# Optimization experiments

Hardware: AMD Instinct MI355X
Metric: run time of the kernel (lower is better)

The kernel has to match this reference:

```python
import jax, jax.numpy as jnp
import numpy as np

B, S, V, D, H, L = 2, 1024, 32000, 1024, 16, 4
DK = D // H
DF = 4 * D
EPS = 1e-5


def setup_inputs() -> dict:
    key = jax.random.key(0)
    ks = jax.random.split(key, 9)
    s = 0.02
    rn = lambda k, shape: jax.random.normal(k, shape, jnp.float32) * s
    return {
        "input_ids": jax.random.randint(ks[0], (B, S), 0, V, dtype=jnp.int32),
        "emb": rn(ks[1], (V, D)),
        "Wq": rn(ks[2], (L, D, D)),
        "Wk": rn(ks[3], (L, D, D)),
        "Wv": rn(ks[4], (L, D, D)),
        "Wo": rn(ks[5], (L, D, D)),
        "W1": rn(ks[6], (L, D, DF)),
        "b1": jnp.zeros((L, DF), jnp.float32),
        "W2": rn(ks[7], (L, DF, D)),
        "b2": jnp.zeros((L, D), jnp.float32),
        "ln1_g": jnp.ones((L, D), jnp.float32),
        "ln1_b": jnp.zeros((L, D), jnp.float32),
        "ln2_g": jnp.ones((L, D), jnp.float32),
        "ln2_b": jnp.zeros((L, D), jnp.float32),
        "lnf_g": jnp.ones((D,), jnp.float32),
        "lnf_b": jnp.zeros((D,), jnp.float32),
        "head_w": rn(ks[8], (D, V)),
    }


def _ln(x, g, b):
    m = jnp.mean(x, -1, keepdims=True)
    v = jnp.mean(jnp.square(x - m), -1, keepdims=True)
    return (x - m) * jax.lax.rsqrt(v + EPS) * g + b


def _heads(x):
    # [B,S,D] -> [B,H,S,DK]
    return x.reshape(B, S, H, DK).transpose(0, 2, 1, 3)


def _forward(input_ids, emb, Wq, Wk, Wv, Wo, W1, b1, W2, b2,
             ln1_g, ln1_b, ln2_g, ln2_b, lnf_g, lnf_b, head_w):
    x = emb[input_ids]  # [B,S,D]
    # causal mask: position q attends to k <= q (prefill, no past)
    mask = jnp.triu(jnp.full((S, S), -jnp.inf, jnp.float32), k=1)
    scale = 1.0 / np.sqrt(DK).astype(np.float32)

    def block(x, p):
        wq, wk, wv, wo, w1, bb1, w2, bb2, g1, be1, g2, be2 = p
        h = _ln(x, g1, be1)
        q = _heads(h @ wq)
        k = _heads(h @ wk)
        v = _heads(h @ wv)
        scores = jnp.einsum('bhqd,bhkd->bhqk', q, k) * scale + mask
        a = jax.nn.softmax(scores, axis=-1)
        o = jnp.einsum('bhqk,bhkd->bhqd', a, v)
        o = o.transpose(0, 2, 1, 3).reshape(B, S, D) @ wo
        x = x + o
        h2 = _ln(x, g2, be2)
        x = x + jax.nn.gelu(h2 @ w1 + bb1, approximate=False) @ w2 + bb2
        return x, None

    x, _ = jax.lax.scan(block, x, (Wq, Wk, Wv, Wo, W1, b1, W2, b2,
                                   ln1_g, ln1_b, ln2_g, ln2_b))
    logits = _ln(x, lnf_g, lnf_b) @ head_w  # [B,S,V]
    return logits


def reference(input_ids, emb, Wq, Wk, Wv, Wo, W1, b1, W2, b2,
              ln1_g, ln1_b, ln2_g, ln2_b, lnf_g, lnf_b, head_w):
    return _forward(input_ids, emb, Wq, Wk, Wv, Wo, W1, b1, W2, b2,
                    ln1_g, ln1_b, ln2_g, ln2_b, lnf_g, lnf_b, head_w)
```

## Files before the change

### kernel.cpp

```cpp
#include <hip/hip_runtime.h>
#include <stdint.h>

#define B_ 2
#define S_ 1024
#define V_ 32000
#define D_ 1024
#define H_ 16
#define L_ 4
#define DF_ 4096
#define M_ (B_*S_)

typedef short short8 __attribute__((ext_vector_type(8)));
typedef float f32x4 __attribute__((ext_vector_type(4)));

__device__ __forceinline__ unsigned short f2bf(float f){
  union { float f; unsigned int u; } v; v.f = f;
  unsigned int u = v.u;
  u = u + 0x7fffu + ((u >> 16) & 1u);
  return (unsigned short)(u >> 16);
}

__device__ __forceinline__ void gload16(const void* g, void* l){
  __builtin_amdgcn_global_load_lds(
      (__attribute__((address_space(1))) void*)(uintptr_t)g,
      (__attribute__((address_space(3))) void*)(uintptr_t)l, 16, 0, 0);
}

__global__ __launch_bounds__(256) void embed_k(const int* __restrict__ ids,
    const float* __restrict__ emb, float* __restrict__ x){
  int row = blockIdx.x;
  int id = ids[row];
  float4 v = reinterpret_cast<const float4*>(emb + (size_t)id*D_)[threadIdx.x];
  reinterpret_cast<float4*>(x + (size_t)row*D_)[threadIdx.x] = v;
}

__global__ __launch_bounds__(256) void ln_k(const float* __restrict__ x,
    const float* __restrict__ g, const float* __restrict__ b,
    unsigned short* __restrict__ out){
  int row = blockIdx.x;
  int tid = threadIdx.x;
  float4 v = reinterpret_cast<const float4*>(x + (size_t)row*D_)[tid];
  float s = v.x+v.y+v.z+v.w;
  float ss = v.x*v.x + v.y*v.y + v.z*v.z + v.w*v.w;
  #pragma unroll
  for (int off=1; off<64; off<<=1){ s += __shfl_xor(s, off); ss += __shfl_xor(ss, off); }
  __shared__ float rs[4], rss[4];
  int wave = tid>>6, lane = tid&63;
  if (lane==0){ rs[wave]=s; rss[wave]=ss; }
  __syncthreads();
  s  = rs[0]+rs[1]+rs[2]+rs[3];
  ss = rss[0]+rss[1]+rss[2]+rss[3];
  float mean = s * (1.0f/(float)D_);
  float var  = ss * (1.0f/(float)D_) - mean*mean;
  float inv = rsqrtf(var + 1e-5f);
  float4 gg = reinterpret_cast<const float4*>(g)[tid];
  float4 bb = reinterpret_cast<const float4*>(b)[tid];
  ushort4 o;
  o.x = f2bf((v.x-mean)*inv*gg.x + bb.x);
  o.y = f2bf((v.y-mean)*inv*gg.y + bb.y);
  o.z = f2bf((v.z-mean)*inv*gg.z + bb.z);
  o.w = f2bf((v.w-mean)*inv*gg.w + bb.w);
  reinterpret_cast<ushort4*>(out + (size_t)row*D_)[tid] = o;
}

__global__ __launch_bounds__(256) void rln_k(float* __restrict__ x,
    const float* __restrict__ part, const float* __restrict__ bias,
    const float* __restrict__ g, const float* __restrict__ b,
    unsigned short* __restrict__ out, int KS){
  int row = blockIdx.x;
  int tid = threadIdx.x;
  float4 v = reinterpret_cast<const float4*>(x + (size_t)row*D_)[tid];
  for (int z=0; z<KS; z++){
    float4 p = reinterpret_cast<const float4*>(part + (size_t)z*M_*D_ + (size_t)row*D_)[tid];
    v.x+=p.x; v.y+=p.y; v.z+=p.z; v.w+=p.w;
  }
  if (bias){
    float4 bb4 = reinterpret_cast<const float4*>(bias)[tid];
    v.x+=bb4.x; v.y+=bb4.y; v.z+=bb4.z; v.w+=bb4.w;
  }
  reinterpret_cast<float4*>(x + (size_t)row*D_)[tid] = v;
  float s = v.x+v.y+v.z+v.w;
  float ss = v.x*v.x + v.y*v.y + v.z*v.z + v.w*v.w;
  #pragma unroll
  for (int off=1; off<64; off<<=1){ s += __shfl_xor(s, off); ss += __shfl_xor(ss, off); }
  __shared__ float rs[4], rss[4];
  int wave = tid>>6, lane = tid&63;
  if (lane==0){ rs[wave]=s; rss[wave]=ss; }
  __syncthreads();
  s  = rs[0]+rs[1]+rs[2]+rs[3];
  ss = rss[0]+rss[1]+rss[2]+rss[3];
  float mean = s * (1.0f/(float)D_);
  float var  = ss * (1.0f/(float)D_) - mean*mean;
  float inv = rsqrtf(var + 1e-5f);
  float4 gg = reinterpret_cast<const float4*>(g)[tid];
  float4 bb = reinterpret_cast<const float4*>(b)[tid];
  ushort4 o;
  o.x = f2bf((v.x-mean)*inv*gg.x + bb.x);
  o.y = f2bf((v.y-mean)*inv*gg.y + bb.y);
  o.z = f2bf((v.z-mean)*inv*gg.z + bb.z);
  o.w = f2bf((v.w-mean)*inv*gg.w + bb.w);
  reinterpret_cast<ushort4*>(out + (size_t)row*D_)[tid] = o;
}

__global__ __launch_bounds__(256) void transpose_k(const float* __restrict__ in,
    unsigned short* __restrict__ out, int K, int N, size_t in_ls, size_t out_ls){
  __shared__ float t[64][65];
  const float* inp = in + (size_t)blockIdx.z*in_ls;
  unsigned short* outp = out + (size_t)blockIdx.z*out_ls;
  int k0 = blockIdx.y*64, n0 = blockIdx.x*64;
  int rr = threadIdx.x >> 4, c4 = (threadIdx.x & 15)*4;
  #pragma unroll
  for (int i=0;i<4;i++){
    float4 v = *reinterpret_cast<const float4*>(inp + (size_t)(k0+rr+i*16)*N + n0 + c4);
    t[rr+i*16][c4+0]=v.x; t[rr+i*16][c4+1]=v.y; t[rr+i*16][c4+2]=v.z; t[rr+i*16][c4+3]=v.w;
  }
  __syncthreads();
  #pragma unroll
  for (int i=0;i<4;i++){
    int n = rr + i*16;
    ushort4 o;
    o.x = f2bf(t[c4+0][n]); o.y = f2bf(t[c4+1][n]);
    o.z = f2bf(t[c4+2][n]); o.w = f2bf(t[c4+3][n]);
    *reinterpret_cast<ushort4*>(outp + (size_t)(n0+n)*K + k0 + c4) = o;
  }
}

#define VMC(n)  asm volatile("s_waitcnt vmcnt(" #n ")" ::: "memory")

template<int EP>
__global__ __launch_bounds__(256)
void gemm_bt(const unsigned short* __restrict__ A, const unsigned short* __restrict__ B,
             void* __restrict__ C, const float* __restrict__ bias,
             const float* __restrict__ resid, int K, int ldc, int MB, int kLen){
  __shared__ unsigned short As[2][128*64];
  __shared__ unsigned short Bs[2][128*64];
  const int tid = threadIdx.x;
  const int wave = tid>>6, lane = tid&63;
  const int wm = wave>>1, wn = wave&1;
  const int nwg = gridDim.x;
  const int p = blockIdx.x;
  const int t = (nwg & 7) ? p : ((p & 7)*(nwg>>3) + (p>>3));
  const int by = t % MB, bx = t / MB;
  const int row0 = by*128, col0 = bx*128;
  const int kz = blockIdx.z;
  const int k0 = kz*kLen;
  f32x4 acc[4][4] = {};
  const int sw8 = ((lane&7) ^ ((lane>>3)&7))*8;
  const unsigned short* Ag = A + (size_t)(row0 + wave*8 + (lane>>3))*K + sw8;
  const unsigned short* Bg = B + (size_t)(col0 + wave*8 + (lane>>3))*K + sw8;
  const int r = lane&15, g16 = lane>>4;
  const int rsw = (r&7)<<4;
#define STAGE_BT(buf, kt) do{ \
    _Pragma("unroll") \
    for (int i=0;i<4;i++){ \
      gload16(Ag + (size_t)i*32*K + (kt), As[buf] + (wave*8 + i*32)*64); \
      gload16(Bg + (size_t)i*32*K + (kt), Bs[buf] + (wave*8 + i*32)*64); \
    } }while(0)
  STAGE_BT(0, k0);
  __syncthreads();
  int cur = 0;
  for (int kt=k0; kt<k0+kLen; kt+=64){
    if (kt + 64 < k0 + kLen) STAGE_BT(cur^1, kt+64);
    #pragma unroll
    for (int ks=0; ks<2; ks++){
      short8 a[4], b[4];
      #pragma unroll
      for (int m=0;m<4;m++)
        a[m] = *reinterpret_cast<const short8*>((const char*)As[cur] + (wm*64+m*16+r)*128 + ((ks*64 + g16*16) ^ rsw));
      #pragma unroll
      for (int n=0;n<4;n++)
        b[n] = *reinterpret_cast<const short8*>((const char*)Bs[cur] + (wn*64+n*16+r)*128 + ((ks*64 + g16*16) ^ rsw));
      #pragma unroll
      for (int m=0;m<4;m++)
        #pragma unroll
        for (int n=0;n<4;n++)
          acc[m][n] = __builtin_amdgcn_mfma_f32_16x16x32_bf16(a[m], b[n], acc[m][n], 0,0,0);
    }
    __syncthreads();
    cur ^= 1;
  }
  #pragma unroll
  for (int m=0;m<4;m++){
    const int row = row0 + wm*64 + m*16 + g16*4;
    #pragma unroll
    for (int n=0;n<4;n++){
      const int col = col0 + wn*64 + n*16 + r;
      #pragma unroll
      for (int j=0;j<4;j++){
        float val = acc[m][n][j];
        size_t idx = (size_t)(row+j)*ldc + col;
        if constexpr (EP==2 || EP==3) val += bias[col];
        if constexpr (EP==2) val = 0.5f*val*(1.0f + erff(val*0.70710678118f));
        if constexpr (EP==1 || EP==3) val += resid[idx];
        if constexpr (EP==0 || EP==2) ((unsigned short*)C)[idx] = f2bf(val);
        else ((float*)C)[idx] = val;
      }
    }
  }
}

#define LDA8(buf,m,ks) (*(const short8*)(lds8 + (buf)*65536 + (wm*128+(m)*16+r)*128 + (((ks)*64+g16*16)^rsw)))
#define LDB8(buf,n,ks) (*(const short8*)(lds8 + (buf)*65536 + 32768 + (wn*64+(n)*16+r)*128 + (((ks)*64+g16*16)^rsw)))
#define STG(buf,isB,h,i,tile) gload16( \
    ((isB) ? Bw + (size_t)(col0 + (h)*128 + (i)*64 + wave*8 + srow)*K + (size_t)(tile)*64 + scsw \
           : A  + (size_t)(row0 + (h)*128 + (i)*64 + wave*8 + srow)*K + (size_t)(tile)*64 + scsw), \
    lds8 + (buf)*65536 + (isB)*32768 + ((h)*128 + (i)*64 + wave*8)*128 )
#define STG_HT(buf,isB,h,tile) do{ STG(buf,isB,h,0,tile); STG(buf,isB,h,1,tile); }while(0)
#define BLOAD8(bT) do{ \
  bfr[0][0]=LDB8(bT,0,0); bfr[0][1]=LDB8(bT,0,1); bfr[1][0]=LDB8(bT,1,0); bfr[1][1]=LDB8(bT,1,1); \
  bfr[2][0]=LDB8(bT,2,0); bfr[2][1]=LDB8(bT,2,1); bfr[3][0]=LDB8(bT,3,0); bfr[3][1]=LDB8(bT,3,1); }while(0)
#define MM8(mb,n) do{ \
  acc[mb][n]    =__builtin_amdgcn_mfma_f32_16x16x32_bf16(a0[0],bfr[n][0],acc[mb][n],0,0,0); \
  acc[mb][n]    =__builtin_amdgcn_mfma_f32_16x16x32_bf16(a0[1],bfr[n][1],acc[mb][n],0,0,0); \
  acc[(mb)+1][n]=__builtin_amdgcn_mfma_f32_16x16x32_bf16(a1[0],bfr[n][0],acc[(mb)+1][n],0,0,0); \
  acc[(mb)+1][n]=__builtin_amdgcn_mfma_f32_16x16x32_bf16(a1[1],bfr[n][1],acc[(mb)+1][n],0,0,0); }while(0)
#define PH8(bT, mb, STAGES, TAIL) do{ \
  short8 a0[2], a1[2]; \
  a0[0]=LDA8(bT,mb,0); a0[1]=LDA8(bT,mb,1); a1[0]=LDA8(bT,(mb)+1,0); a1[1]=LDA8(bT,(mb)+1,1); \
  STAGES; \
  __builtin_amdgcn_s_barrier(); \
  asm volatile("s_waitcnt lgkmcnt(0)" ::: "memory"); \
  __builtin_amdgcn_s_setprio(1); \
  MM8(mb,0); MM8(mb,1); MM8(mb,2); MM8(mb,3); \
  __builtin_amdgcn_s_setprio(0); \
  TAIL; \
  __builtin_amdgcn_s_barrier(); \
}while(0)

__global__ __launch_bounds__(512, 2)
void gemm_8ph(const unsigned short* __restrict__ A, const unsigned short* __restrict__ Bw,
              float* __restrict__ C, int K, int ldc, int MB){
  __shared__ char lds8[131072];
  const int tid = threadIdx.x;
  const int wave = tid>>6, lane = tid&63;
  const int wm = wave>>2, wn = wave&3;
  const int nwg = gridDim.x;
  const int pp = blockIdx.x;
  const int t = (nwg & 7) ? pp : ((pp & 7)*(nwg>>3) + (pp>>3));
  const int by = t % MB, bx = t / MB;
  const int row0 = by*256, col0 = bx*256;
  const int r = lane&15, g16 = lane>>4;
  const int rsw = (r&7)<<4;
  const int srow = lane>>3;
  const int scsw = ((lane&7) ^ srow)*8;

  f32x4 acc[8][4] = {};
  short8 bfr[4][2];
  const int NT = K/64;

  STG_HT(0,1,0,0); STG_HT(0,1,1,0);
  STG_HT(0,0,0,0); STG_HT(0,0,1,0);
  STG_HT(1,1,0,1); STG_HT(1,1,1,1);
  VMC(4);
  __builtin_amdgcn_s_barrier();

  for (int T0 = 0; T0 < NT-2; T0 += 2){
    BLOAD8(0);
    PH8(0, 0, STG_HT(1,0,0,T0+1), ((void)0));
    PH8(0, 2, STG_HT(1,0,1,T0+1), ((void)0));
    PH8(0, 4, STG_HT(0,1,0,T0+2), ((void)0));
    PH8(0, 6, STG_HT(0,1,1,T0+2), VMC(4));
    BLOAD8(1);
    PH8(1, 0, STG_HT(0,0,0,T0+2), ((void)0));
    PH8(1, 2, STG_HT(0,0,1,T0+2), ((void)0));
    PH8(1, 4, STG_HT(1,1,0,T0+3), ((void)0));
    PH8(1, 6, STG_HT(1,1,1,T0+3), VMC(4));
  }
  BLOAD8(0);
  PH8(0, 0, STG_HT(1,0,0,NT-1), ((void)0));
  PH8(0, 2, STG_HT(1,0,1,NT-1), ((void)0));
  PH8(0, 4, ((void)0), ((void)0));
  PH8(0, 6, ((void)0), VMC(0));
  BLOAD8(1);
  PH8(1, 0, ((void)0), ((void)0));
  PH8(1, 2, ((void)0), ((void)0));
  PH8(1, 4, ((void)0), ((void)0));
  PH8(1, 6, ((void)0), ((void)0));

  #pragma unroll
  for (int m=0;m<8;m++){
    const int row = row0 + wm*128 + m*16 + g16*4;
    #pragma unroll
    for (int n=0;n<4;n++){
      const int col = col0 + wn*64 + n*16 + r;
      #pragma unroll
      for (int j=0;j<4;j++)
        C[(size_t)(row+j)*ldc + col] = acc[m][n][j];
    }
  }
}

#define L4A(buf,m,ks) (*(const short8*)(lds4 + (buf)*49152 + (wm*64+(m)*16+r)*128 + (((ks)*64+g16*16)^rsw)))
#define L4B(buf,n,ks) (*(const short8*)(lds4 + (buf)*49152 + 16384 + (wn*64+(n)*16+r)*128 + (((ks)*64+g16*16)^rsw)))
#define STG4A(buf,tile) do{ \
  gload16(A4 + (size_t)(row0 + 0*64 + wave*8 + srow)*K + (size_t)(tile)*64 + scsw, lds4 + (buf)*49152 + (0*64+wave*8)*128); \
  gload16(A4 + (size_t)(row0 + 1*64 + wave*8 + srow)*K + (size_t)(tile)*64 + scsw, lds4 + (buf)*49152 + (1*64+wave*8)*128); }while(0)
#define STG4B(buf,tile) do{ \
  gload16(B4 + (size_t)(col0 + 0*64 + wave*8 + srow)*K + (size_t)(tile)*64 + scsw, lds4 + (buf)*49152 + 16384 + (0*64+wave*8)*128); \
  gload16(B4 + (size_t)(col0 + 1*64 + wave*8 + srow)*K + (size_t)(tile)*64 + scsw, lds4 + (buf)*49152 + 16384 + (1*64+wave*8)*128); \
  gload16(B4 + (size_t)(col0 + 2*64 + wave*8 + srow)*K + (size_t)(tile)*64 + scsw, lds4 + (buf)*49152 + 16384 + (2*64+wave*8)*128); \
  gload16(B4 + (size_t)(col0 + 3*64 + wave*8 + srow)*K + (size_t)(tile)*64 + scsw, lds4 + (buf)*49152 + 16384 + (3*64+wave*8)*128); }while(0)
#define BLOAD4(bT) do{ \
  bfr4[0][0]=L4B(bT,0,0); bfr4[0][1]=L4B(bT,0,1); bfr4[1][0]=L4B(bT,1,0); bfr4[1][1]=L4B(bT,1,1); \
  bfr4[2][0]=L4B(bT,2,0); bfr4[2][1]=L4B(bT,2,1); bfr4[3][0]=L4B(bT,3,0); bfr4[3][1]=L4B(bT,3,1); }while(0)
#define MM44(mb,n) do{ \
  acc[mb][n]    =__builtin_amdgcn_mfma_f32_16x16x32_bf16(a0[0],bfr4[n][0],acc[mb][n],0,0,0); \
  acc[mb][n]    =__builtin_amdgcn_mfma_f32_16x16x32_bf16(a0[1],bfr4[n][1],acc[mb][n],0,0,0); \
  acc[(mb)+1][n]=__builtin_amdgcn_mfma_f32_16x16x32_bf16(a1[0],bfr4[n][0],acc[(mb)+1][n],0,0,0); \
  acc[(mb)+1][n]=__builtin_amdgcn_mfma_f32_16x16x32_bf16(a1[1],bfr4[n][1],acc[(mb)+1][n],0,0,0); }while(0)
#define PH4(bT, mb, STAGES, TAIL) do{ \
  short8 a0[2], a1[2]; \
  a0[0]=L4A(bT,mb,0); a0[1]=L4A(bT,mb,1); a1[0]=L4A(bT,(mb)+1,0); a1[1]=L4A(bT,(mb)+1,1); \
  STAGES; \
  __builtin_amdgcn_s_barrier(); \
  asm volatile("s_waitcnt lgkmcnt(0)" ::: "memory"); \
  __builtin_amdgcn_s_setprio(1); \
  MM44(mb,0); MM44(mb,1); MM44(mb,2); MM44(mb,3); \
  __builtin_amdgcn_s_setprio(0); \
  TAIL; \
  __builtin_amdgcn_s_barrier(); \
}while(0)

template<int EP>
__global__ __launch_bounds__(512, 2)
void gemm_4ph(const unsigned short* __restrict__ A, const unsigned short* __restrict__ Bw,
              void* __restrict__ C, const float* __restrict__ bias,
              int K, int ldc, int MB, int kLen){
  __shared__ char lds4[98304];
  const int tid = threadIdx.x;
  const int wave = tid>>6, lane = tid&63;
  const int wm = wave>>2, wn = wave&3;
  const int nwg = gridDim.x;
  const int pp = blockIdx.x;
  const int t = (nwg & 7) ? pp : ((pp & 7)*(nwg>>3) + (pp>>3));
  const int by = t % MB, bx = t / MB;
  const int row0 = by*128, col0 = bx*256;
  const int r = lane&15, g16 = lane>>4;
  const int rsw = (r&7)<<4;
  const int srow = lane>>3;
  const int scsw = ((lane&7) ^ srow)*8;
  const int kz = blockIdx.z;
  const unsigned short* A4 = A + (size_t)kz*kLen;
  const unsigned short* B4 = Bw + (size_t)kz*kLen;

  f32x4 acc[4][4] = {};
  short8 bfr4[4][2];
  const int NT = kLen/64;

  STG4B(0,0); STG4A(0,0); STG4B(1,1);
  VMC(4);
  __builtin_amdgcn_s_barrier();

  for (int T0 = 0; T0 < NT-2; T0 += 2){
    BLOAD4(0);
    PH4(0, 0, STG4A(1,T0+1), ((void)0));
    PH4(0, 2, STG4B(0,T0+2), VMC(4));
    BLOAD4(1);
    PH4(1, 0, STG4A(0,T0+2), ((void)0));
    PH4(1, 2, STG4B(1,T0+3), VMC(4));
  }
  BLOAD4(0);
  PH4(0, 0, STG4A(1,NT-1), ((void)0));
  PH4(0, 2, ((void)0), VMC(0));
  BLOAD4(1);
  PH4(1, 0, ((void)0), ((void)0));
  PH4(1, 2, ((void)0), ((void)0));

  float* Cp5 = (float*)C + (size_t)kz*M_*ldc;
  #pragma unroll
  for (int m=0;m<4;m++){
    const int row = row0 + wm*64 + m*16 + g16*4;
    #pragma unroll
    for (int n=0;n<4;n++){
      const int col = col0 + wn*64 + n*16 + r;
      #pragma unroll
      for (int j=0;j<4;j++){
        float val = acc[m][n][j];
        size_t idx = (size_t)(row+j)*ldc + col;
        if constexpr (EP==2) { val += bias[col]; val = 0.5f*val*(1.0f + erff(val*0.70710678118f)); }
        if constexpr (EP==0 || EP==2) ((unsigned short*)C)[idx] = f2bf(val);
        else Cp5[idx] = val;
      }
    }
  }
}

__global__ __launch_bounds__(256)
void attn_k(const unsigned short* __restrict__ qkv, unsigned short* __restrict__ o){
  __shared__ unsigned short Ks[64*64];
  __shared__ unsigned short Vt[64*64];
  __shared__ unsigned short Ps[4*16*64];
  const int tid = threadIdx.x;
  const int wave = tid>>6, lane = tid&63;
  const int qb = blockIdx.x, h = blockIdx.y, b = blockIdx.z;
  const int r = lane&15, g = lane>>4;
  const size_t rowbase = (size_t)b*S_*3*D_;
  short8 qf[2];
  {
    const unsigned short* qp = qkv + rowbase + (size_t)(qb*64 + wave*16 + r)*(3*D_) + h*64 + g*8;
    qf[0] = *reinterpret_cast<const short8*>(qp);
    qf[1] = *reinterpret_cast<const short8*>(qp + 32);
  }
  float mrow[4] = {-INFINITY,-INFINITY,-INFINITY,-INFINITY};
  float lrow[4] = {0.f,0.f,0.f,0.f};
  f32x4 oacc[4] = {};
  const int qglob0 = qb*64 + wave*16 + g*4;
  unsigned short* Pw = Ps + wave*16*64;

  for (int kt=0; kt<=qb; kt++){
    __syncthreads();
    #pragma unroll
    for (int i=0;i<2;i++){
      int key = i*32 + (tid>>3);
      int c8 = (tid&7)*8;
      const unsigned short* kp = qkv + rowbase + (size_t)(kt*64+key)*(3*D_) + D_ + h*64 + c8;
      uint4 kd = *reinterpret_cast<const uint4*>(kp);
      int bo = (key*128 + c8*2) ^ ((key&7)<<4);
      *reinterpret_cast<uint4*>((char*)Ks + bo) = kd;
      const unsigned short* vp = qkv + rowbase + (size_t)(kt*64+key)*(3*D_) + 2*D_ + h*64 + c8;
      uint4 vd = *reinterpret_cast<const uint4*>(vp);
      const unsigned short* ve = reinterpret_cast<const unsigned short*>(&vd);
      #pragma unroll
      for (int j=0;j<8;j++){
        int d = c8 + j;
        int bo2 = (d*128 + key*2) ^ ((d&7)<<4);
        *reinterpret_cast<unsigned short*>((char*)Vt + bo2) = ve[j];
      }
    }
    __syncthreads();
    f32x4 sacc[4] = {};
    #pragma unroll
    for (int ks=0; ks<2; ks++){
      #pragma unroll
      for (int nb=0; nb<4; nb++){
        int key = nb*16 + r;
        int bo = (key*128 + (ks*32+g*8)*2) ^ ((key&7)<<4);
        short8 kf = *reinterpret_cast<const short8*>((char*)Ks + bo);
        sacc[nb] = __builtin_amdgcn_mfma_f32_16x16x32_bf16(qf[ks], kf, sacc[nb], 0,0,0);
      }
    }
    float sv[4][4];
    float tm[4] = {-INFINITY,-INFINITY,-INFINITY,-INFINITY};
    #pragma unroll
    for (int nb=0; nb<4; nb++){
      int key = kt*64 + nb*16 + r;
      #pragma unroll
      for (int j=0;j<4;j++){
        float s = sacc[nb][j]*0.125f;
        s = (key <= qglob0 + j) ? s : -INFINITY;
        sv[nb][j] = s;
        tm[j] = fmaxf(tm[j], s);
      }
    }
    #pragma unroll
    for (int off=1; off<16; off<<=1){
      #pragma unroll
      for (int j=0;j<4;j++) tm[j] = fmaxf(tm[j], __shfl_xor(tm[j], off));
    }
    float sf[4], psum[4];
    #pragma unroll
    for (int j=0;j<4;j++){
      float mn = fmaxf(mrow[j], tm[j]);
      sf[j] = __expf(mrow[j]-mn);
      mrow[j] = mn;
      psum[j] = 0.0f;
    }
    #pragma unroll
    for (int nb=0; nb<4; nb++){
      #pragma unroll
      for (int j=0;j<4;j++){
        float p = __expf(sv[nb][j]-mrow[j]);
        psum[j] += p;
        int prow = g*4+j;
        int bo = (prow*128 + (nb*16+r)*2) ^ ((prow&7)<<4);
        *reinterpret_cast<unsigned short*>((char*)Pw + bo) = f2bf(p);
      }
    }
    #pragma unroll
    for (int off=1; off<16; off<<=1){
      #pragma unroll
      for (int j=0;j<4;j++) psum[j] += __shfl_xor(psum[j], off);
    }
    #pragma unroll
    for (int j=0;j<4;j++) lrow[j] = lrow[j]*sf[j] + psum[j];
    #pragma unroll
    for (int nb=0;nb<4;nb++){
      #pragma unroll
      for (int j=0;j<4;j++) oacc[nb][j] *= sf[j];
    }
    asm volatile("s_waitcnt lgkmcnt(0)" ::: "memory");
    #pragma unroll
    for (int ks=0; ks<2; ks++){
      int bo = (r*128 + (ks*32+g*8)*2) ^ ((r&7)<<4);
      short8 pf = *reinterpret_cast<const short8*>((char*)Pw + bo);
      #pragma unroll
      for (int nb=0; nb<4; nb++){
        int d = nb*16 + r;
        int bo2 = (d*128 + (ks*32+g*8)*2) ^ ((d&7)<<4);
        short8 vf = *reinterpret_cast<const short8*>((char*)Vt + bo2);
        oacc[nb] = __builtin_amdgcn_mfma_f32_16x16x32_bf16(pf, vf, oacc[nb], 0,0,0);
      }
    }
  }
  #pragma unroll
  for (int nb=0; nb<4; nb++){
    #pragma unroll
    for (int j=0;j<4;j++){
      float ov = oacc[nb][j] / lrow[j];
      size_t row = (size_t)b*S_ + qb*64 + wave*16 + g*4 + j;
      o[row*D_ + h*64 + nb*16 + r] = f2bf(ov);
    }
  }
}

extern "C" void kernel_launch(void* const* d_in, const int* in_sizes, int n_in,
                              void* d_out, int out_size, void* d_ws, size_t ws_size,
                              hipStream_t stream) {
  const int*   ids   = (const int*)  d_in[0];
  const float* emb   = (const float*)d_in[1];
  const float* Wq    = (const float*)d_in[2];
  const float* Wk    = (const float*)d_in[3];
  const float* Wv    = (const float*)d_in[4];
  const float* Wo    = (const float*)d_in[5];
  const float* W1    = (const float*)d_in[6];
  const float* b1    = (const float*)d_in[7];
  const float* W2    = (const float*)d_in[8];
  const float* b2    = (const float*)d_in[9];
  const float* ln1_g = (const float*)d_in[10];
  const float* ln1_b = (const float*)d_in[11];
  const float* ln2_g = (const float*)d_in[12];
  const float* ln2_b = (const float*)d_in[13];
  const float* lnf_g = (const float*)d_in[14];
  const float* lnf_b = (const float*)d_in[15];
  const float* headw = (const float*)d_in[16];

  unsigned short* ws = (unsigned short*)d_ws;
  unsigned short* wqkvT = ws;
  unsigned short* woT   = wqkvT + (size_t)L_*3*D_*D_;
  unsigned short* w1T   = woT   + (size_t)L_*D_*D_;
  unsigned short* w2T   = w1T   + (size_t)L_*D_*DF_;
  unsigned short* headT = w2T   + (size_t)L_*D_*DF_;
  unsigned short* h     = headT + (size_t)V_*D_;
  unsigned short* qkv   = h     + (size_t)M_*D_;
  unsigned short* attno = qkv   + (size_t)M_*3*D_;
  unsigned short* h2    = attno + (size_t)M_*D_;
  float*          x     = (float*)(h2 + (size_t)M_*DF_);
  float*          part  = x + (size_t)M_*D_;
  size_t needed = ((char*)(part + (size_t)4*M_*D_)) - (char*)d_ws;
  const bool splitk = (ws_size >= needed);

  transpose_k<<<dim3(D_/64, D_/64, L_), 256, 0, stream>>>(Wq, wqkvT,            D_, D_, (size_t)D_*D_, (size_t)3*D_*D_);
  transpose_k<<<dim3(D_/64, D_/64, L_), 256, 0, stream>>>(Wk, wqkvT + D_*D_,    D_, D_, (size_t)D_*D_, (size_t)3*D_*D_);
  transpose_k<<<dim3(D_/64, D_/64, L_), 256, 0, stream>>>(Wv, wqkvT + 2*D_*D_,  D_, D_, (size_t)D_*D_, (size_t)3*D_*D_);
  transpose_k<<<dim3(D_/64, D_/64, L_), 256, 0, stream>>>(Wo, woT,              D_, D_, (size_t)D_*D_, (size_t)D_*D_);
  transpose_k<<<dim3(DF_/64, D_/64, L_), 256, 0, stream>>>(W1, w1T,             D_, DF_, (size_t)D_*DF_, (size_t)D_*DF_);
  transpose_k<<<dim3(D_/64, DF_/64, L_), 256, 0, stream>>>(W2, w2T,             DF_, D_, (size_t)D_*DF_, (size_t)D_*DF_);
  transpose_k<<<dim3(V_/64, D_/64, 1), 256, 0, stream>>>(headw, headT,          D_, V_, 0, 0);

  embed_k<<<M_, 256, 0, stream>>>(ids, emb, x);
  ln_k<<<M_, 256, 0, stream>>>(x, ln1_g, ln1_b, h);

  for (int l = 0; l < L_; l++){
    gemm_4ph<0><<<dim3((3*D_/256)*(M_/128), 1, 1), 512, 0, stream>>>(h, wqkvT + (size_t)l*3*D_*D_, qkv, nullptr, D_, 3*D_, M_/128, D_);
    attn_k<<<dim3(S_/64, H_, B_), 256, 0, stream>>>(qkv, attno);
    if (splitk){
      gemm_4ph<5><<<dim3((D_/256)*(M_/128), 1, 4), 512, 0, stream>>>(attno, woT + (size_t)l*D_*D_, part, nullptr, D_, D_, M_/128, D_/4);
      rln_k<<<M_, 256, 0, stream>>>(x, part, nullptr, ln2_g + l*D_, ln2_b + l*D_, h, 4);
    } else {
      gemm_bt<1><<<dim3((D_/128)*(M_/128), 1, 1), 256, 0, stream>>>(attno, woT + (size_t)l*D_*D_, x, nullptr, x, D_, D_, M_/128, D_);
      ln_k<<<M_, 256, 0, stream>>>(x, ln2_g + l*D_, ln2_b + l*D_, h);
    }
    gemm_4ph<2><<<dim3((DF_/256)*(M_/128), 1, 1), 512, 0, stream>>>(h, w1T + (size_t)l*D_*DF_, h2, b1 + l*DF_, D_, DF_, M_/128, D_);
    const float* ng = (l+1 < L_) ? (ln1_g + (l+1)*D_) : lnf_g;
    const float* nb = (l+1 < L_) ? (ln1_b + (l+1)*D_) : lnf_b;
    if (splitk){
      gemm_4ph<5><<<dim3((D_/256)*(M_/128), 1, 4), 512, 0, stream>>>(h2, w2T + (size_t)l*D_*DF_, part, nullptr, DF_, D_, M_/128, DF_/4);
      rln_k<<<M_, 256, 0, stream>>>(x, part, b2 + l*D_, ng, nb, h, 4);
    } else {
      gemm_bt<3><<<dim3((D_/128)*(M_/128), 1, 1), 256, 0, stream>>>(h2, w2T + (size_t)l*D_*DF_, x, b2 + l*D_, x, DF_, D_, M_/128, DF_);
      ln_k<<<M_, 256, 0, stream>>>(x, ng, nb, h);
    }
  }

  gemm_8ph<<<dim3((V_/256)*(M_/256), 1, 1), 512, 0, stream>>>(h, headT, (float*)d_out, D_, V_, M_/256);
}
```

Measured before the change: 894.1 us.

## Double-buffer K/V tiles in attention and skip redundant rescaling

The attention kernel now double-buffers K and V tiles in shared memory. It prefetches the next K tile with direct global-to-LDS loads and the next V tile into registers while computing on the current tile, so the loads overlap the MFMA and softmax work. The 1/sqrt(dk) scale is folded into Q at load time, the causal mask is applied only on the diagonal tile, and the running-max rescale of the output and row sum is skipped when no row max changed. This doubles the K/V shared-memory footprint, which may lower occupancy, and rounding the scaled Q to bf16 slightly changes numerics.

```diff
diff --git a/kernel.cpp b/kernel.cpp
--- a/kernel.cpp
+++ b/kernel.cpp
@@ -18,6 +18,11 @@
   unsigned int u = v.u;
   u = u + 0x7fffu + ((u >> 16) & 1u);
   return (unsigned short)(u >> 16);
+}
+
+__device__ __forceinline__ float bf2f(unsigned short u){
+  union { unsigned int u; float f; } v; v.u = ((unsigned int)u) << 16;
+  return v.f;
 }
 
 __device__ __forceinline__ void gload16(const void* g, void* l){
@@ -387,47 +392,69 @@
 
 __global__ __launch_bounds__(256)
 void attn_k(const unsigned short* __restrict__ qkv, unsigned short* __restrict__ o){
-  __shared__ unsigned short Ks[64*64];
-  __shared__ unsigned short Vt[64*64];
+  __shared__ unsigned short Ks[2][64*64];
+  __shared__ unsigned short Vt[2][64*64];
   __shared__ unsigned short Ps[4*16*64];
   const int tid = threadIdx.x;
   const int wave = tid>>6, lane = tid&63;
   const int qb = blockIdx.x, h = blockIdx.y, b = blockIdx.z;
   const int r = lane&15, g = lane>>4;
   const size_t rowbase = (size_t)b*S_*3*D_;
+  const unsigned short* kbase = qkv + rowbase + D_ + h*64;
+  const unsigned short* vbase = qkv + rowbase + 2*D_ + h*64;
   short8 qf[2];
   {
     const unsigned short* qp = qkv + rowbase + (size_t)(qb*64 + wave*16 + r)*(3*D_) + h*64 + g*8;
-    qf[0] = *reinterpret_cast<const short8*>(qp);
-    qf[1] = *reinterpret_cast<const short8*>(qp + 32);
+    short8 q0 = *reinterpret_cast<const short8*>(qp);
+    short8 q1 = *reinterpret_cast<const short8*>(qp + 32);
+    #pragma unroll
+    for (int j=0;j<8;j++){
+      qf[0][j] = (short)f2bf(bf2f((unsigned short)q0[j])*0.125f);
+      qf[1][j] = (short)f2bf(bf2f((unsigned short)q1[j])*0.125f);
+    }
   }
   float mrow[4] = {-INFINITY,-INFINITY,-INFINITY,-INFINITY};
   float lrow[4] = {0.f,0.f,0.f,0.f};
   f32x4 oacc[4] = {};
   const int qglob0 = qb*64 + wave*16 + g*4;
   unsigned short* Pw = Ps + wave*16*64;
-
+  uint4 vdr[2];
+
+  const int key8 = tid>>3;
+  const int c8   = (tid&7)*8;
+  const int kcsw = ((tid&7) ^ (key8&7))*16;
+
+#define KSTG_A(nxt, kt2) do{ \
+  gload16((const char*)(kbase + (size_t)((kt2)*64+key8)*(3*D_)) + kcsw, (char*)Ks[nxt] + wave*1024); \
+  gload16((const char*)(kbase + (size_t)((kt2)*64+32+key8)*(3*D_)) + kcsw, (char*)Ks[nxt] + 4096 + wave*1024); \
+}while(0)
+#define VLOAD_A(kt2) do{ \
+  vdr[0] = *reinterpret_cast<const uint4*>(vbase + (size_t)((kt2)*64+key8)*(3*D_) + c8); \
+  vdr[1] = *reinterpret_cast<const uint4*>(vbase + (size_t)((kt2)*64+32+key8)*(3*D_) + c8); \
+}while(0)
+#define VSTORE_A(nxt) do{ \
+  _Pragma("unroll") \
+  for (int i=0;i<2;i++){ \
+    int key = i*32 + key8; \
+    const unsigned short* ve = reinterpret_cast<const unsigned short*>(&vdr[i]); \
+    _Pragma("unroll") \
+    for (int j=0;j<8;j++){ \
+      int d = c8 + j; \
+      int bo2 = (d*128 + key*2) ^ ((d&7)<<4); \
+      *reinterpret_cast<unsigned short*>((char*)Vt[nxt] + bo2) = ve[j]; \
+    } \
+  } }while(0)
+
+  KSTG_A(0, 0);
+  VLOAD_A(0);
+  VMC(0);
+  VSTORE_A(0);
+  __syncthreads();
+
+  int cur = 0;
   for (int kt=0; kt<=qb; kt++){
-    __syncthreads();
-    #pragma unroll
-    for (int i=0;i<2;i++){
-      int key = i*32 + (tid>>3);
-      int c8 = (tid&7)*8;
-      const unsigned short* kp = qkv + rowbase + (size_t)(kt*64+key)*(3*D_) + D_ + h*64 + c8;
-      uint4 kd = *reinterpret_cast<const uint4*>(kp);
-      int bo = (key*128 + c8*2) ^ ((key&7)<<4);
-      *reinterpret_cast<uint4*>((char*)Ks + bo) = kd;
-      const unsigned short* vp = qkv + rowbase + (size_t)(kt*64+key)*(3*D_) + 2*D_ + h*64 + c8;
-      uint4 vd = *reinterpret_cast<const uint4*>(vp);
-      const unsigned short* ve = reinterpret_cast<const unsigned short*>(&vd);
-      #pragma unroll
-      for (int j=0;j<8;j++){
-        int d = c8 + j;
-        int bo2 = (d*128 + key*2) ^ ((d&7)<<4);
-        *reinterpret_cast<unsigned short*>((char*)Vt + bo2) = ve[j];
-      }
-    }
-    __syncthreads();
+    const bool pf = (kt < qb);
+    if (pf){ KSTG_A(cur^1, kt+1); VLOAD_A(kt+1); }
     f32x4 sacc[4] = {};
     #pragma unroll
     for (int ks=0; ks<2; ks++){
@@ -435,36 +462,53 @@
       for (int nb=0; nb<4; nb++){
         int key = nb*16 + r;
         int bo = (key*128 + (ks*32+g*8)*2) ^ ((key&7)<<4);
-        short8 kf = *reinterpret_cast<const short8*>((char*)Ks + bo);
+        short8 kf = *reinterpret_cast<const short8*>((char*)Ks[cur] + bo);
         sacc[nb] = __builtin_amdgcn_mfma_f32_16x16x32_bf16(qf[ks], kf, sacc[nb], 0,0,0);
       }
     }
     float sv[4][4];
     float tm[4] = {-INFINITY,-INFINITY,-INFINITY,-INFINITY};
-    #pragma unroll
-    for (int nb=0; nb<4; nb++){
-      int key = kt*64 + nb*16 + r;
+    if (kt == qb){
+      #pragma unroll
+      for (int nb=0; nb<4; nb++){
+        int key = kt*64 + nb*16 + r;
+        #pragma unroll
+        for (int j=0;j<4;j++){
+          float s = (key <= qglob0 + j) ? sacc[nb][j] : -INFINITY;
+          sv[nb][j] = s;
+          tm[j] = fmaxf(tm[j], s);
+        }
+      }
+    } else {
+      #pragma unroll
+      for (int nb=0; nb<4; nb++)
+        #pragma unroll
+        for (int j=0;j<4;j++){
+          float s = sacc[nb][j];
+          sv[nb][j] = s;
+          tm[j] = fmaxf(tm[j], s);
+        }
+    }
+    #pragma unroll
+    for (int off=1; off<16; off<<=1){
+      #pragma unroll
+      for (int j=0;j<4;j++) tm[j] = fmaxf(tm[j], __shfl_xor(tm[j], off));
+    }
+    int chg = 0;
+    float mn[4];
+    #pragma unroll
+    for (int j=0;j<4;j++){ mn[j] = fmaxf(mrow[j], tm[j]); chg |= (mn[j] > mrow[j]); }
+    if (__any(chg)){
       #pragma unroll
       for (int j=0;j<4;j++){
-        float s = sacc[nb][j]*0.125f;
-        s = (key <= qglob0 + j) ? s : -INFINITY;
-        sv[nb][j] = s;
-        tm[j] = fmaxf(tm[j], s);
+        float sf = __expf(mrow[j]-mn[j]);
+        mrow[j] = mn[j];
+        lrow[j] *= sf;
+        #pragma unroll
+        for (int nb=0;nb<4;nb++) oacc[nb][j] *= sf;
       }
     }
-    #pragma unroll
-    for (int off=1; off<16; off<<=1){
-      #pragma unroll
-      for (int j=0;j<4;j++) tm[j] = fmaxf(tm[j], __shfl_xor(tm[j], off));
-    }
-    float sf[4], psum[4];
-    #pragma unroll
-    for (int j=0;j<4;j++){
-      float mn = fmaxf(mrow[j], tm[j]);
-      sf[j] = __expf(mrow[j]-mn);
-      mrow[j] = mn;
-      psum[j] = 0.0f;
-    }
+    float psum[4] = {0.f,0.f,0.f,0.f};
     #pragma unroll
     for (int nb=0; nb<4; nb++){
       #pragma unroll
@@ -482,25 +526,23 @@
       for (int j=0;j<4;j++) psum[j] += __shfl_xor(psum[j], off);
     }
     #pragma unroll
-    for (int j=0;j<4;j++) lrow[j] = lrow[j]*sf[j] + psum[j];
-    #pragma unroll
-    for (int nb=0;nb<4;nb++){
-      #pragma unroll
-      for (int j=0;j<4;j++) oacc[nb][j] *= sf[j];
-    }
+    for (int j=0;j<4;j++) lrow[j] += psum[j];
     asm volatile("s_waitcnt lgkmcnt(0)" ::: "memory");
     #pragma unroll
     for (int ks=0; ks<2; ks++){
       int bo = (r*128 + (ks*32+g*8)*2) ^ ((r&7)<<4);
-      short8 pf = *reinterpret_cast<const short8*>((char*)Pw + bo);
+      short8 pf8 = *reinterpret_cast<const short8*>((char*)Pw + bo);
       #pragma unroll
       for (int nb=0; nb<4; nb++){
         int d = nb*16 + r;
         int bo2 = (d*128 + (ks*32+g*8)*2) ^ ((d&7)<<4);
-        short8 vf = *reinterpret_cast<const short8*>((char*)Vt + bo2);
-        oacc[nb] = __builtin_amdgcn_mfma_f32_16x16x32_bf16(pf, vf, oacc[nb], 0,0,0);
+        short8 vf = *reinterpret_cast<const short8*>((char*)Vt[cur] + bo2);
+        oacc[nb] = __builtin_amdgcn_mfma_f32_16x16x32_bf16(pf8, vf, oacc[nb], 0,0,0);
       }
     }
+    if (pf){ VMC(0); VSTORE_A(cur^1); }
+    __syncthreads();
+    cur ^= 1;
   }
   #pragma unroll
   for (int nb=0; nb<4; nb++){
```

After: 893.9 us, median of 2. Within noise of the previous version (-0.0%).
